# Kernel tuning notes

Measured on AMD Instinct MI355X. Metric: run time of the kernel, lower is better.

Reference implementation:

```python
import jax, jax.numpy as jnp
import numpy as np

# Dims: B=32 batch, C=64 feat channels, Np=192 priors, No=72 row offsets,
# Ns=36 pooled sample points (maxpool kernel 2), Hd=64 fc hidden.
B, C, Np, No, Hd = 32, 64, 192, 72, 64
NS_POOL = 2  # n_offsets // sample_points
REG_DIM = No + 4  # reg_layers output


def bilinear_sample(feat, gx, gy):
    """torch F.grid_sample(align_corners=True) equivalent for in-range coords.
    feat: [B,C,H,W]; gx,gy: [B,Np,S] normalized to [-1,1]. -> [B,C,Np,S]."""
    Bb, Cc, H, W = feat.shape
    ix = (gx + 1.0) * 0.5 * (W - 1)
    iy = (gy + 1.0) * 0.5 * (H - 1)
    ix0f = jnp.floor(ix); iy0f = jnp.floor(iy)
    wx = ix - ix0f; wy = iy - iy0f
    ix0 = jnp.clip(ix0f.astype(jnp.int32), 0, W - 1)
    iy0 = jnp.clip(iy0f.astype(jnp.int32), 0, H - 1)
    ix1 = jnp.clip(ix0 + 1, 0, W - 1)
    iy1 = jnp.clip(iy0 + 1, 0, H - 1)
    ff = feat.reshape(Bb, Cc, H * W)
    S = gx.shape[1] * gx.shape[2]
    def gather(iy_, ix_):
        idx = (iy_ * W + ix_).reshape(Bb, 1, S)
        g = jnp.take_along_axis(ff, jnp.broadcast_to(idx, (Bb, Cc, S)), axis=2)
        return g.reshape(Bb, Cc, gx.shape[1], gx.shape[2])
    v00 = gather(iy0, ix0); v01 = gather(iy0, ix1)
    v10 = gather(iy1, ix0); v11 = gather(iy1, ix1)
    wx = wx[:, None]; wy = wy[:, None]  # broadcast over C
    return (v00 * (1 - wx) * (1 - wy) + v01 * wx * (1 - wy)
            + v10 * (1 - wx) * wy + v11 * wx * wy)


def _mlp2(h, Ws, bs):
    # two stacked Linear+ReLU layers (num_fc=2)
    for i in range(2):
        h = jax.nn.relu(h @ Ws[i] + bs[i])
    return h


def setup_inputs() -> dict:
    key = jax.random.key(0)
    ks = jax.random.split(key, 24)
    w = lambda k, sh: jax.random.normal(k, sh, dtype=jnp.float32) * 0.05
    return {
        "x0": jax.random.normal(ks[0], (B, C, 40, 100), dtype=jnp.float32),
        "x1": jax.random.normal(ks[1], (B, C, 20, 50), dtype=jnp.float32),
        "x2": jax.random.normal(ks[2], (B, C, 10, 25), dtype=jnp.float32),
        "prior_xs0": jax.random.uniform(ks[3], (Np, No), dtype=jnp.float32),
        "l_weight": w(ks[4], (No,)),              # self.l embedding, sigmoid gate
        "lsgi_w": w(ks[5], (3, C, C)),            # per-stage lsgi projection
        "fc_w": w(ks[6], (C, Hd)), "fc_b": w(ks[7], (Hd,)),
        "cls_w": w(ks[8], (2, Hd, Hd)), "cls_b": w(ks[9], (2, Hd)),
        "cls_ow": w(ks[10], (Hd, 2)), "cls_ob": w(ks[11], (2,)),
        "reg_w": w(ks[12], (2, Hd, Hd)), "reg_b": w(ks[13], (2, Hd)),
        "reg_ow": w(ks[14], (Hd, REG_DIM)), "reg_ob": w(ks[15], (REG_DIM,)),
        "loc_w": w(ks[16], (2, Hd, Hd)), "loc_b": w(ks[17], (2, Hd)),
        "loc_ow": w(ks[18], (Hd, 1)), "loc_ob": w(ks[19], (1,)),
    }


def reference(x0, x1, x2, prior_xs0, l_weight, lsgi_w, fc_w, fc_b,
              cls_w, cls_b, cls_ow, cls_ob, reg_w, reg_b, reg_ow, reg_ob,
              loc_w, loc_b, loc_ow, loc_ob):
    pyramid = [x2, x1, x0]  # reversed: coarsest level first (stage 0)
    prior_feat_ys = jnp.linspace(1.0, 0.0, No, dtype=jnp.float32)
    gy = jnp.broadcast_to((prior_feat_ys * 2.0 - 1.0)[None, None, :], (B, Np, No))
    prior_xs = jnp.broadcast_to(prior_xs0[None], (B, Np, No))
    gate = jax.nn.sigmoid(l_weight)[:, None]  # [No,1]
    stage_feats = []
    outs = []
    for s in range(3):
        gx = prior_xs * 2.0 - 1.0
        pooled = bilinear_sample(pyramid[s], gx, gy)          # [B,C,Np,No]
        pooled = jnp.transpose(pooled, (0, 2, 3, 1)) * gate   # [B,Np,No,C]
        pooled = jax.nn.relu(jnp.einsum('bnoc,cd->bnod', pooled, lsgi_w[s]))
        # MaxPool2d kernel (2,1) over the offset axis -> Ns=36 sample points
        comp = pooled.reshape(B, Np, No // NS_POOL, NS_POOL, C).max(axis=3)
        stage_feats.append(comp)
        # cross-stage fusion (global head): mean over stages and sample points
        fused = jnp.stack(stage_feats, 0).mean(axis=0).mean(axis=2)  # [B,Np,C]
        fc = jax.nn.relu(fused @ fc_w + fc_b)                        # [B,Np,Hd]
        cls = _mlp2(fc, cls_w, cls_b) @ cls_ow + cls_ob              # [B,Np,2]
        reg = _mlp2(fc, reg_w, reg_b) @ reg_ow + reg_ob              # [B,Np,No+4]
        loc = _mlp2(fc, loc_w, loc_b) @ loc_ow + loc_ob              # [B,Np,1]
        outs.append(jnp.concatenate([cls, reg, loc], axis=-1))      # [B,Np,79]
        # refine anchors for next stage from predicted xs
        prior_xs = jax.nn.sigmoid(reg[..., 4:])
    return jnp.stack(outs, axis=0)  # [3,B,Np,79]
```

## Files before the change

### kernel.cpp

```cpp
#include <hip/hip_runtime.h>
#include <hip/hip_bf16.h>

#define Bq   32
#define Cq   64
#define NPq  192
#define NOq  72
#define PTS  (NPq * NOq)
#define REGD 76
#define OUTD 79
#define HSTR 68

typedef __attribute__((ext_vector_type(8))) short short8;
typedef __attribute__((ext_vector_type(4))) float float4v;

__device__ inline unsigned short f2bf(float x) {
    __hip_bfloat16 h = __float2bfloat16(x);
    return *reinterpret_cast<unsigned short*>(&h);
}
__device__ inline float bf2f(unsigned short u) {
    unsigned int x = ((unsigned int)u) << 16;
    float f;
    __builtin_memcpy(&f, &x, 4);
    return f;
}

__global__ __launch_bounds__(256) void build_tables_kernel(
    const float* __restrict__ f0,
    const float* __restrict__ f1,
    const float* __restrict__ f2,
    const float* __restrict__ lw,
    unsigned short* __restrict__ t0,
    unsigned short* __restrict__ t1,
    unsigned short* __restrict__ t2)
{
    __shared__ float sRow[64 * 101];

    const int tid = threadIdx.x;
    const int o   = blockIdx.x / 96;
    const int sb  = blockIdx.x - o * 96;
    const int s   = sb >> 5;
    const int b   = sb & 31;

    const float* feat; unsigned short* tab; int H, W;
    if (s == 0)      { feat = f0; tab = t0; H = 10; W = 25; }
    else if (s == 1) { feat = f1; tab = t1; H = 20; W = 50; }
    else             { feat = f2; tab = t2; H = 40; W = 100; }
    const int Wp = W + 1;

    const float ys = 1.0f - (float)o * (1.0f / 71.0f);
    const float iy = ys * (float)(H - 1);
    const float fy = floorf(iy);
    const float wy = iy - fy;
    int iy0 = (int)fy; iy0 = iy0 < 0 ? 0 : (iy0 > H - 1 ? H - 1 : iy0);
    const int iy1 = (iy0 + 1 > H - 1) ? H - 1 : iy0 + 1;
    const float gate = 1.0f / (1.0f + __expf(-lw[o]));

    const float* fb = feat + (size_t)b * 64 * H * W;
    const int iy0W = iy0 * W, iy1W = iy1 * W;

    const int tot = 64 * W;
    for (int idx = tid; idx < tot; idx += 256) {
        const int c = idx / W;
        const int x = idx - c * W;
        const float* f = fb + c * (H * W);
        sRow[c * Wp + x] = ((1.0f - wy) * f[iy0W + x] + wy * f[iy1W + x]) * gate;
    }
    __syncthreads();

    unsigned short* to = tab + (size_t)(b * NOq + o) * Wp * 64;
    const int tot2 = Wp * 64;
    for (int idx = tid; idx < tot2; idx += 256) {
        const int x = idx >> 6;
        const int c = idx & 63;
        const int xx = (x < W) ? x : (W - 1);
        to[idx] = f2bf(sRow[c * Wp + xx]);
    }
}

template<int W>
__global__ __launch_bounds__(256) void fused_pool_kernel(
    const unsigned short* __restrict__ tab,
    const float* __restrict__ xsrc, const int xstride,
    const float* __restrict__ lsgi,
    float* __restrict__ sumFeat,
    const int accumulate)
{
    constexpr int Wp = W + 1;
    const int tid  = threadIdx.x;
    const int w    = tid >> 6;
    const int lane = tid & 63;
    const int ng   = blockIdx.x >> 5;
    const int b    = blockIdx.x & 31;
    const int npair = ng * 4 + w;

    short8 wf[4][2];
    {
        const int kb = ((lane >> 4) & 3) * 8;
        const int dl = lane & 15;
        #pragma unroll
        for (int ks = 0; ks < 2; ++ks)
            #pragma unroll
            for (int dt = 0; dt < 4; ++dt) {
                union { unsigned short u[8]; short8 v; } pk;
                #pragma unroll
                for (int j = 0; j < 8; ++j)
                    pk.u[j] = f2bf(lsgi[(ks * 32 + kb + j) * 64 + dt * 16 + dl]);
                wf[dt][ks] = pk.v;
            }
    }

    const unsigned short* tb = tab + (size_t)b * NOq * Wp * 64;
    const float* xp = xsrc + (size_t)xstride * b;
    const int m  = lane & 15;
    const int kg = lane >> 4;
    const int nt0 = npair * 9;

    float sums0[4] = {0.f, 0.f, 0.f, 0.f};
    float sums1[4] = {0.f, 0.f, 0.f, 0.f};

    #pragma unroll
    for (int ntl = 0; ntl < 9; ++ntl) {
        const int pt = (nt0 + ntl) * 16 + m;
        const int o  = pt % NOq;
        float ixf = xp[pt] * (float)(W - 1);
        ixf = fminf(fmaxf(ixf, 0.0f), (float)(W - 1));
        const float fx = floorf(ixf);
        const float wx = ixf - fx;
        const int ix0 = (int)fx;

        const unsigned short* col = tb + ((size_t)o * Wp + ix0) * 64 + kg * 8;
        union { unsigned short u[8]; short8 v; } t00, t01, t10, t11, a0, a1;
        t00.v = *(const short8*)(col);
        t01.v = *(const short8*)(col + 64);
        t10.v = *(const short8*)(col + 32);
        t11.v = *(const short8*)(col + 96);
        #pragma unroll
        for (int j = 0; j < 8; ++j) {
            const float l0 = bf2f(t00.u[j]), h0 = bf2f(t01.u[j]);
            const float l1 = bf2f(t10.u[j]), h1 = bf2f(t11.u[j]);
            a0.u[j] = f2bf(l0 + wx * (h0 - l0));
            a1.u[j] = f2bf(l1 + wx * (h1 - l1));
        }

        const bool hi = (ntl * 16 + (kg * 4)) >= NOq;
        #pragma unroll
        for (int dt = 0; dt < 4; ++dt) {
            float4v c = {0.f, 0.f, 0.f, 0.f};
            c = __builtin_amdgcn_mfma_f32_16x16x32_bf16(a0.v, wf[dt][0], c, 0, 0, 0);
            c = __builtin_amdgcn_mfma_f32_16x16x32_bf16(a1.v, wf[dt][1], c, 0, 0, 0);
            const float pm0 = fmaxf(fmaxf(c[0], c[1]), 0.f);
            const float pm1 = fmaxf(fmaxf(c[2], c[3]), 0.f);
            const float add = pm0 + pm1;
            if (hi) sums1[dt] += add; else sums0[dt] += add;
        }
    }

    #pragma unroll
    for (int dt = 0; dt < 4; ++dt) {
        float v0 = sums0[dt], v1 = sums1[dt];
        v0 += __shfl_xor(v0, 16); v0 += __shfl_xor(v0, 32);
        v1 += __shfl_xor(v1, 16); v1 += __shfl_xor(v1, 32);
        sums0[dt] = v0; sums1[dt] = v1;
    }

    if (lane < 16) {
        const size_t row0 = (size_t)(b * NPq + npair * 2) * 64;
        #pragma unroll
        for (int dt = 0; dt < 4; ++dt) {
            const int d = dt * 16 + lane;
            float t0 = sums0[dt] * (1.0f / 36.0f);
            float t1 = sums1[dt] * (1.0f / 36.0f);
            float* p0 = sumFeat + row0 + d;
            float* p1 = sumFeat + row0 + 64 + d;
            if (accumulate) { t0 += *p0; t1 += *p1; }
            *p0 = t0; *p1 = t1;
        }
    }
}

__global__ __launch_bounds__(256) void head_kernel(
    const float* __restrict__ sumFeat, const float invS,
    const float* __restrict__ fc_w,  const float* __restrict__ fc_b,
    const float* __restrict__ cls_w, const float* __restrict__ cls_b,
    const float* __restrict__ cls_ow, const float* __restrict__ cls_ob,
    const float* __restrict__ reg_w, const float* __restrict__ reg_b,
    const float* __restrict__ reg_ow, const float* __restrict__ reg_ob,
    const float* __restrict__ loc_w, const float* __restrict__ loc_b,
    const float* __restrict__ loc_ow, const float* __restrict__ loc_ob,
    float* __restrict__ out, float* __restrict__ xs_next)
{
    __shared__ __align__(16) float sAct0[32 * HSTR];
    __shared__ __align__(16) float sAct1[32 * HSTR];
    __shared__ __align__(16) float sW0[4096];
    __shared__ __align__(16) float sW1[4864];

    const int tid = threadIdx.x;
    const int hb  = blockIdx.x % 3;
    const int pg  = blockIdx.x / 3;
    const int p0  = pg * 32;
    const int tm  = tid >> 4;
    const int tn  = tid & 15;

    const float* h_w  = (hb == 0) ? cls_w  : (hb == 1) ? reg_w  : loc_w;
    const float* h_b  = (hb == 0) ? cls_b  : (hb == 1) ? reg_b  : loc_b;
    const float* h_ow = (hb == 0) ? cls_ow : (hb == 1) ? reg_ow : loc_ow;
    const float* h_ob = (hb == 0) ? cls_ob : (hb == 1) ? reg_ob : loc_ob;
    const int ow_n    = (hb == 0) ? 128    : (hb == 1) ? 64 * REGD : 64;

    #pragma unroll
    for (int i = 0; i < 4; ++i)
        *(float4*)&sW0[(i * 256 + tid) * 4] = *(const float4*)&fc_w[(i * 256 + tid) * 4];
    for (int idx = tid; idx < 32 * 64; idx += 256) {
        const int p = idx >> 6, c = idx & 63;
        sAct0[p * HSTR + c] = sumFeat[(size_t)(p0 + p) * 64 + c] * invS;
    }

    auto do_gemm = [&](const float* src, float* dst, const float* wbuf,
                       const float* gb, const float* nextw, int nextn,
                       float* nextbuf) {
        __syncthreads();
        float4 pf[5];
        const int n4 = nextn >> 2;
        #pragma unroll
        for (int i = 0; i < 5; ++i) {
            const int idx = i * 256 + tid;
            if (idx < n4) pf[i] = *(const float4*)&nextw[idx * 4];
        }
        const float4 b4 = *(const float4*)&gb[4 * tn];
        float4 acc0 = b4, acc1 = b4;
        const float* r0 = src + (2 * tm) * HSTR;
        const float* r1 = r0 + HSTR;
        #pragma unroll 4
        for (int k4 = 0; k4 < 16; ++k4) {
            const float4 a0 = *(const float4*)&r0[4 * k4];
            const float4 a1 = *(const float4*)&r1[4 * k4];
            const float4 w0 = *(const float4*)&wbuf[(4 * k4 + 0) * 64 + 4 * tn];
            const float4 w1 = *(const float4*)&wbuf[(4 * k4 + 1) * 64 + 4 * tn];
            const float4 w2 = *(const float4*)&wbuf[(4 * k4 + 2) * 64 + 4 * tn];
            const float4 w3 = *(const float4*)&wbuf[(4 * k4 + 3) * 64 + 4 * tn];
            acc0.x += a0.x*w0.x + a0.y*w1.x + a0.z*w2.x + a0.w*w3.x;
            acc0.y += a0.x*w0.y + a0.y*w1.y + a0.z*w2.y + a0.w*w3.y;
            acc0.z += a0.x*w0.z + a0.y*w1.z + a0.z*w2.z + a0.w*w3.z;
            acc0.w += a0.x*w0.w + a0.y*w1.w + a0.z*w2.w + a0.w*w3.w;
            acc1.x += a1.x*w0.x + a1.y*w1.x + a1.z*w2.x + a1.w*w3.x;
            acc1.y += a1.x*w0.y + a1.y*w1.y + a1.z*w2.y + a1.w*w3.y;
            acc1.z += a1.x*w0.z + a1.y*w1.z + a1.z*w2.z + a1.w*w3.z;
            acc1.w += a1.x*w0.w + a1.y*w1.w + a1.z*w2.w + a1.w*w3.w;
        }
        float4 v0, v1;
        v0.x = fmaxf(acc0.x, 0.f); v0.y = fmaxf(acc0.y, 0.f);
        v0.z = fmaxf(acc0.z, 0.f); v0.w = fmaxf(acc0.w, 0.f);
        v1.x = fmaxf(acc1.x, 0.f); v1.y = fmaxf(acc1.y, 0.f);
        v1.z = fmaxf(acc1.z, 0.f); v1.w = fmaxf(acc1.w, 0.f);
        *(float4*)&dst[(2 * tm) * HSTR + 4 * tn]     = v0;
        *(float4*)&dst[(2 * tm + 1) * HSTR + 4 * tn] = v1;
        #pragma unroll
        for (int i = 0; i < 5; ++i) {
            const int idx = i * 256 + tid;
            if (idx < n4) *(float4*)&nextbuf[idx * 4] = pf[i];
        }
    };

    do_gemm(sAct0, sAct1, sW0, fc_b,      h_w,        4096, sW1);
    do_gemm(sAct1, sAct0, sW1, h_b,       h_w + 4096, 4096, sW0);
    do_gemm(sAct0, sAct1, sW0, h_b + 64,  h_ow,       ow_n, sW1);
    __syncthreads();

    if (hb == 0) {
        if (tid < 64) {
            const int p = tid >> 1, d = tid & 1;
            const float* row = &sAct1[p * HSTR];
            float z = h_ob[d];
            #pragma unroll 4
            for (int k4 = 0; k4 < 16; ++k4) {
                const float4 a = *(const float4*)&row[4 * k4];
                z += a.x * sW1[(4 * k4 + 0) * 2 + d] + a.y * sW1[(4 * k4 + 1) * 2 + d]
                   + a.z * sW1[(4 * k4 + 2) * 2 + d] + a.w * sW1[(4 * k4 + 3) * 2 + d];
            }
            out[(size_t)(p0 + p) * OUTD + d] = z;
        }
    } else if (hb == 1) {
        const int p  = tid & 31;
        const int jg = tid >> 5;
        const float* row = &sAct1[p * HSTR];
        float* orow = out + (size_t)(p0 + p) * OUTD;
        float* xsp  = xs_next + (size_t)(p0 + p) * NOq;
        for (int j = jg; j < REGD; j += 8) {
            float z = h_ob[j];
            #pragma unroll 4
            for (int k4 = 0; k4 < 16; ++k4) {
                const float4 a = *(const float4*)&row[4 * k4];
                z += a.x * sW1[(4 * k4 + 0) * REGD + j] + a.y * sW1[(4 * k4 + 1) * REGD + j]
                   + a.z * sW1[(4 * k4 + 2) * REGD + j] + a.w * sW1[(4 * k4 + 3) * REGD + j];
            }
            orow[2 + j] = z;
            if (j >= 4) xsp[j - 4] = 1.0f / (1.0f + __expf(-z));
        }
    } else {
        if (tid < 32) {
            const float* row = &sAct1[tid * HSTR];
            float z = h_ob[0];
            #pragma unroll 4
            for (int k4 = 0; k4 < 16; ++k4) {
                const float4 a = *(const float4*)&row[4 * k4];
                z += a.x * sW1[4 * k4] + a.y * sW1[4 * k4 + 1]
                   + a.z * sW1[4 * k4 + 2] + a.w * sW1[4 * k4 + 3];
            }
            out[(size_t)(p0 + tid) * OUTD + 78] = z;
        }
    }
}

extern "C" void kernel_launch(void* const* d_in, const int* in_sizes, int n_in,
                              void* d_out, int out_size, void* d_ws, size_t ws_size,
                              hipStream_t stream)
{
    const float* x0        = (const float*)d_in[0];
    const float* x1        = (const float*)d_in[1];
    const float* x2        = (const float*)d_in[2];
    const float* prior_xs0 = (const float*)d_in[3];
    const float* l_weight  = (const float*)d_in[4];
    const float* lsgi_w    = (const float*)d_in[5];
    const float* fc_w      = (const float*)d_in[6];
    const float* fc_b      = (const float*)d_in[7];
    const float* cls_w     = (const float*)d_in[8];
    const float* cls_b     = (const float*)d_in[9];
    const float* cls_ow    = (const float*)d_in[10];
    const float* cls_ob    = (const float*)d_in[11];
    const float* reg_w     = (const float*)d_in[12];
    const float* reg_b     = (const float*)d_in[13];
    const float* reg_ow    = (const float*)d_in[14];
    const float* reg_ob    = (const float*)d_in[15];
    const float* loc_w     = (const float*)d_in[16];
    const float* loc_b     = (const float*)d_in[17];
    const float* loc_ow    = (const float*)d_in[18];
    const float* loc_ob    = (const float*)d_in[19];

    float* out     = (float*)d_out;
    float* sumFeat = (float*)d_ws;
    float* xs      = sumFeat + (size_t)Bq * NPq * Cq;
    unsigned short* tab0 = (unsigned short*)(xs + (size_t)Bq * PTS);
    unsigned short* tab1 = tab0 + (size_t)Bq * NOq * 26  * 64;
    unsigned short* tab2 = tab1 + (size_t)Bq * NOq * 51  * 64;

    hipLaunchKernelGGL(build_tables_kernel, dim3(3 * Bq * NOq), dim3(256), 0, stream,
                       x2, x1, x0, l_weight, tab0, tab1, tab2);

    for (int s = 0; s < 3; ++s) {
        const float* xsrc = (s == 0) ? prior_xs0 : xs;
        const int xstr    = (s == 0) ? 0 : PTS;
        if (s == 0)
            hipLaunchKernelGGL((fused_pool_kernel<25>), dim3(Bq * 24), dim3(256), 0, stream,
                               tab0, xsrc, xstr, lsgi_w + s * 4096, sumFeat, 0);
        else if (s == 1)
            hipLaunchKernelGGL((fused_pool_kernel<50>), dim3(Bq * 24), dim3(256), 0, stream,
                               tab1, xsrc, xstr, lsgi_w + s * 4096, sumFeat, 1);
        else
            hipLaunchKernelGGL((fused_pool_kernel<100>), dim3(Bq * 24), dim3(256), 0, stream,
                               tab2, xsrc, xstr, lsgi_w + s * 4096, sumFeat, 1);

        hipLaunchKernelGGL(head_kernel, dim3((Bq * NPq / 32) * 3), dim3(256), 0, stream,
                           sumFeat, 1.0f / (float)(s + 1),
                           fc_w, fc_b, cls_w, cls_b, cls_ow, cls_ob,
                           reg_w, reg_b, reg_ow, reg_ob,
                           loc_w, loc_b, loc_ow, loc_ob,
                           out + (size_t)s * Bq * NPq * OUTD, xs);
    }
}
```

Baseline: 279.6 us.

## Fuse head MLPs into pooling kernel and template table build on stage dims

The separate head kernel is folded into the pooling kernel: each block keeps its 8 priors' fused features in shared memory and runs the fc, cls, reg and loc MLPs in place. This removes three launches and the sumFeat reload. The table builder is templated on H/W and writes packed bf16 pairs as 32-bit stores. In exchange, each of the 768 blocks reloads every head weight matrix into shared memory for only 8 rows, with many more barriers and serial GEMM phases. It also uses extra shared memory, which may reduce occupancy of the pooling phase.

```diff
diff --git a/kernel.cpp b/kernel.cpp
--- a/kernel.cpp
+++ b/kernel.cpp
@@ -8,7 +8,6 @@
 #define PTS  (NPq * NOq)
 #define REGD 76
 #define OUTD 79
-#define HSTR 68
 
 typedef __attribute__((ext_vector_type(8))) short short8;
 typedef __attribute__((ext_vector_type(4))) float float4v;
@@ -22,6 +21,46 @@
     float f;
     __builtin_memcpy(&f, &x, 4);
     return f;
+}
+
+template<int H, int W>
+__device__ __forceinline__ void build_one(
+    const float* __restrict__ feat, unsigned short* __restrict__ tab,
+    const float* __restrict__ lw, const int b, const int o,
+    float* __restrict__ sRow, const int tid)
+{
+    constexpr int Wp = W + 1;
+
+    const float ys = 1.0f - (float)o * (1.0f / 71.0f);
+    const float iy = ys * (float)(H - 1);
+    const float fy = floorf(iy);
+    const float wy = iy - fy;
+    int iy0 = (int)fy; iy0 = iy0 < 0 ? 0 : (iy0 > H - 1 ? H - 1 : iy0);
+    const int iy1 = (iy0 + 1 > H - 1) ? H - 1 : iy0 + 1;
+    const float gate = 1.0f / (1.0f + __expf(-lw[o]));
+
+    const float* fb = feat + (size_t)b * 64 * H * W;
+    const int iy0W = iy0 * W, iy1W = iy1 * W;
+
+    constexpr int tot = 64 * W;
+    for (int idx = tid; idx < tot; idx += 256) {
+        const int c = idx / W;
+        const int x = idx - c * W;
+        const float* f = fb + c * (H * W);
+        sRow[c * Wp + x] = ((1.0f - wy) * f[iy0W + x] + wy * f[iy1W + x]) * gate;
+    }
+    __syncthreads();
+
+    unsigned int* to = (unsigned int*)(tab + (size_t)(b * NOq + o) * Wp * 64);
+    constexpr int tot2 = Wp * 32;
+    for (int idx = tid; idx < tot2; idx += 256) {
+        const int x  = idx >> 5;
+        const int c0 = (idx & 31) * 2;
+        const int xx = (x < W) ? x : (W - 1);
+        const unsigned int lo = f2bf(sRow[c0 * Wp + xx]);
+        const unsigned int hi = f2bf(sRow[(c0 + 1) * Wp + xx]);
+        to[x * 32 + (c0 >> 1)] = lo | (hi << 16);
+    }
 }
 
 __global__ __launch_bounds__(256) void build_tables_kernel(
@@ -34,58 +73,40 @@
     unsigned short* __restrict__ t2)
 {
     __shared__ float sRow[64 * 101];
-
     const int tid = threadIdx.x;
     const int o   = blockIdx.x / 96;
     const int sb  = blockIdx.x - o * 96;
     const int s   = sb >> 5;
     const int b   = sb & 31;
 
-    const float* feat; unsigned short* tab; int H, W;
-    if (s == 0)      { feat = f0; tab = t0; H = 10; W = 25; }
-    else if (s == 1) { feat = f1; tab = t1; H = 20; W = 50; }
-    else             { feat = f2; tab = t2; H = 40; W = 100; }
-    const int Wp = W + 1;
-
-    const float ys = 1.0f - (float)o * (1.0f / 71.0f);
-    const float iy = ys * (float)(H - 1);
-    const float fy = floorf(iy);
-    const float wy = iy - fy;
-    int iy0 = (int)fy; iy0 = iy0 < 0 ? 0 : (iy0 > H - 1 ? H - 1 : iy0);
-    const int iy1 = (iy0 + 1 > H - 1) ? H - 1 : iy0 + 1;
-    const float gate = 1.0f / (1.0f + __expf(-lw[o]));
-
-    const float* fb = feat + (size_t)b * 64 * H * W;
-    const int iy0W = iy0 * W, iy1W = iy1 * W;
-
-    const int tot = 64 * W;
-    for (int idx = tid; idx < tot; idx += 256) {
-        const int c = idx / W;
-        const int x = idx - c * W;
-        const float* f = fb + c * (H * W);
-        sRow[c * Wp + x] = ((1.0f - wy) * f[iy0W + x] + wy * f[iy1W + x]) * gate;
-    }
-    __syncthreads();
-
-    unsigned short* to = tab + (size_t)(b * NOq + o) * Wp * 64;
-    const int tot2 = Wp * 64;
-    for (int idx = tid; idx < tot2; idx += 256) {
-        const int x = idx >> 6;
-        const int c = idx & 63;
-        const int xx = (x < W) ? x : (W - 1);
-        to[idx] = f2bf(sRow[c * Wp + xx]);
-    }
+    if (s == 0)      build_one<10, 25 >(f0, t0, lw, b, o, sRow, tid);
+    else if (s == 1) build_one<20, 50 >(f1, t1, lw, b, o, sRow, tid);
+    else             build_one<40, 100>(f2, t2, lw, b, o, sRow, tid);
 }
 
 template<int W>
-__global__ __launch_bounds__(256) void fused_pool_kernel(
+__global__ __launch_bounds__(256) void fused_pool_head_kernel(
     const unsigned short* __restrict__ tab,
     const float* __restrict__ xsrc, const int xstride,
     const float* __restrict__ lsgi,
     float* __restrict__ sumFeat,
-    const int accumulate)
+    const int stage,
+    const float* __restrict__ fc_w,  const float* __restrict__ fc_b,
+    const float* __restrict__ cls_w, const float* __restrict__ cls_b,
+    const float* __restrict__ cls_ow, const float* __restrict__ cls_ob,
+    const float* __restrict__ reg_w, const float* __restrict__ reg_b,
+    const float* __restrict__ reg_ow, const float* __restrict__ reg_ob,
+    const float* __restrict__ loc_w, const float* __restrict__ loc_b,
+    const float* __restrict__ loc_ow, const float* __restrict__ loc_ob,
+    float* __restrict__ out, float* __restrict__ xs_next)
 {
     constexpr int Wp = W + 1;
+    __shared__ __align__(16) float sF [8][68];
+    __shared__ __align__(16) float sC [8][68];
+    __shared__ __align__(16) float sT1[8][68];
+    __shared__ __align__(16) float sT2[8][68];
+    __shared__ __align__(16) float sWt[4864];
+
     const int tid  = threadIdx.x;
     const int w    = tid >> 6;
     const int lane = tid & 63;
@@ -163,6 +184,7 @@
         sums0[dt] = v0; sums1[dt] = v1;
     }
 
+    const float invS = 1.0f / (float)(stage + 1);
     if (lane < 16) {
         const size_t row0 = (size_t)(b * NPq + npair * 2) * 64;
         #pragma unroll
@@ -172,142 +194,74 @@
             float t1 = sums1[dt] * (1.0f / 36.0f);
             float* p0 = sumFeat + row0 + d;
             float* p1 = sumFeat + row0 + 64 + d;
-            if (accumulate) { t0 += *p0; t1 += *p1; }
+            if (stage > 0) { t0 += *p0; t1 += *p1; }
             *p0 = t0; *p1 = t1;
-        }
-    }
-}
-
-__global__ __launch_bounds__(256) void head_kernel(
-    const float* __restrict__ sumFeat, const float invS,
-    const float* __restrict__ fc_w,  const float* __restrict__ fc_b,
-    const float* __restrict__ cls_w, const float* __restrict__ cls_b,
-    const float* __restrict__ cls_ow, const float* __restrict__ cls_ob,
-    const float* __restrict__ reg_w, const float* __restrict__ reg_b,
-    const float* __restrict__ reg_ow, const float* __restrict__ reg_ob,
-    const float* __restrict__ loc_w, const float* __restrict__ loc_b,
-    const float* __restrict__ loc_ow, const float* __restrict__ loc_ob,
-    float* __restrict__ out, float* __restrict__ xs_next)
-{
-    __shared__ __align__(16) float sAct0[32 * HSTR];
-    __shared__ __align__(16) float sAct1[32 * HSTR];
-    __shared__ __align__(16) float sW0[4096];
-    __shared__ __align__(16) float sW1[4864];
-
-    const int tid = threadIdx.x;
-    const int hb  = blockIdx.x % 3;
-    const int pg  = blockIdx.x / 3;
-    const int p0  = pg * 32;
-    const int tm  = tid >> 4;
-    const int tn  = tid & 15;
-
-    const float* h_w  = (hb == 0) ? cls_w  : (hb == 1) ? reg_w  : loc_w;
-    const float* h_b  = (hb == 0) ? cls_b  : (hb == 1) ? reg_b  : loc_b;
-    const float* h_ow = (hb == 0) ? cls_ow : (hb == 1) ? reg_ow : loc_ow;
-    const float* h_ob = (hb == 0) ? cls_ob : (hb == 1) ? reg_ob : loc_ob;
-    const int ow_n    = (hb == 0) ? 128    : (hb == 1) ? 64 * REGD : 64;
-
-    #pragma unroll
-    for (int i = 0; i < 4; ++i)
-        *(float4*)&sW0[(i * 256 + tid) * 4] = *(const float4*)&fc_w[(i * 256 + tid) * 4];
-    for (int idx = tid; idx < 32 * 64; idx += 256) {
-        const int p = idx >> 6, c = idx & 63;
-        sAct0[p * HSTR + c] = sumFeat[(size_t)(p0 + p) * 64 + c] * invS;
-    }
-
-    auto do_gemm = [&](const float* src, float* dst, const float* wbuf,
-                       const float* gb, const float* nextw, int nextn,
-                       float* nextbuf) {
+            sF[2 * w][d]     = t0 * invS;
+            sF[2 * w + 1][d] = t1 * invS;
+        }
+    }
+
+    const int pt2 = tid >> 5;
+    const int dh  = tid & 31;
+    const int d0  = dh * 2;
+    const int p0g = b * NPq + ng * 8;
+
+    auto gemm64 = [&](const float (*src)[68], float (*dst)[68],
+                      const float* __restrict__ gw, const float* __restrict__ gb) {
         __syncthreads();
-        float4 pf[5];
-        const int n4 = nextn >> 2;
-        #pragma unroll
-        for (int i = 0; i < 5; ++i) {
-            const int idx = i * 256 + tid;
-            if (idx < n4) pf[i] = *(const float4*)&nextw[idx * 4];
-        }
-        const float4 b4 = *(const float4*)&gb[4 * tn];
-        float4 acc0 = b4, acc1 = b4;
-        const float* r0 = src + (2 * tm) * HSTR;
-        const float* r1 = r0 + HSTR;
-        #pragma unroll 4
-        for (int k4 = 0; k4 < 16; ++k4) {
-            const float4 a0 = *(const float4*)&r0[4 * k4];
-            const float4 a1 = *(const float4*)&r1[4 * k4];
-            const float4 w0 = *(const float4*)&wbuf[(4 * k4 + 0) * 64 + 4 * tn];
-            const float4 w1 = *(const float4*)&wbuf[(4 * k4 + 1) * 64 + 4 * tn];
-            const float4 w2 = *(const float4*)&wbuf[(4 * k4 + 2) * 64 + 4 * tn];
-            const float4 w3 = *(const float4*)&wbuf[(4 * k4 + 3) * 64 + 4 * tn];
-            acc0.x += a0.x*w0.x + a0.y*w1.x + a0.z*w2.x + a0.w*w3.x;
-            acc0.y += a0.x*w0.y + a0.y*w1.y + a0.z*w2.y + a0.w*w3.y;
-            acc0.z += a0.x*w0.z + a0.y*w1.z + a0.z*w2.z + a0.w*w3.z;
-            acc0.w += a0.x*w0.w + a0.y*w1.w + a0.z*w2.w + a0.w*w3.w;
-            acc1.x += a1.x*w0.x + a1.y*w1.x + a1.z*w2.x + a1.w*w3.x;
-            acc1.y += a1.x*w0.y + a1.y*w1.y + a1.z*w2.y + a1.w*w3.y;
-            acc1.z += a1.x*w0.z + a1.y*w1.z + a1.z*w2.z + a1.w*w3.z;
-            acc1.w += a1.x*w0.w + a1.y*w1.w + a1.z*w2.w + a1.w*w3.w;
-        }
-        float4 v0, v1;
-        v0.x = fmaxf(acc0.x, 0.f); v0.y = fmaxf(acc0.y, 0.f);
-        v0.z = fmaxf(acc0.z, 0.f); v0.w = fmaxf(acc0.w, 0.f);
-        v1.x = fmaxf(acc1.x, 0.f); v1.y = fmaxf(acc1.y, 0.f);
-        v1.z = fmaxf(acc1.z, 0.f); v1.w = fmaxf(acc1.w, 0.f);
-        *(float4*)&dst[(2 * tm) * HSTR + 4 * tn]     = v0;
-        *(float4*)&dst[(2 * tm + 1) * HSTR + 4 * tn] = v1;
-        #pragma unroll
-        for (int i = 0; i < 5; ++i) {
-            const int idx = i * 256 + tid;
-            if (idx < n4) *(float4*)&nextbuf[idx * 4] = pf[i];
-        }
+        #pragma unroll
+        for (int i = 0; i < 4; ++i)
+            *(float4*)&sWt[(i * 256 + tid) * 4] = *(const float4*)&gw[(i * 256 + tid) * 4];
+        __syncthreads();
+        float a0 = gb[d0], a1 = gb[d0 + 1];
+        #pragma unroll 8
+        for (int k = 0; k < 64; ++k) {
+            const float av = src[pt2][k];
+            const float2 w2 = *(const float2*)&sWt[k * 64 + d0];
+            a0 += av * w2.x; a1 += av * w2.y;
+        }
+        dst[pt2][d0]     = fmaxf(a0, 0.f);
+        dst[pt2][d0 + 1] = fmaxf(a1, 0.f);
     };
 
-    do_gemm(sAct0, sAct1, sW0, fc_b,      h_w,        4096, sW1);
-    do_gemm(sAct1, sAct0, sW1, h_b,       h_w + 4096, 4096, sW0);
-    do_gemm(sAct0, sAct1, sW0, h_b + 64,  h_ow,       ow_n, sW1);
-    __syncthreads();
-
-    if (hb == 0) {
-        if (tid < 64) {
-            const int p = tid >> 1, d = tid & 1;
-            const float* row = &sAct1[p * HSTR];
-            float z = h_ob[d];
-            #pragma unroll 4
-            for (int k4 = 0; k4 < 16; ++k4) {
-                const float4 a = *(const float4*)&row[4 * k4];
-                z += a.x * sW1[(4 * k4 + 0) * 2 + d] + a.y * sW1[(4 * k4 + 1) * 2 + d]
-                   + a.z * sW1[(4 * k4 + 2) * 2 + d] + a.w * sW1[(4 * k4 + 3) * 2 + d];
-            }
-            out[(size_t)(p0 + p) * OUTD + d] = z;
-        }
-    } else if (hb == 1) {
-        const int p  = tid & 31;
-        const int jg = tid >> 5;
-        const float* row = &sAct1[p * HSTR];
-        float* orow = out + (size_t)(p0 + p) * OUTD;
-        float* xsp  = xs_next + (size_t)(p0 + p) * NOq;
-        for (int j = jg; j < REGD; j += 8) {
-            float z = h_ob[j];
-            #pragma unroll 4
-            for (int k4 = 0; k4 < 16; ++k4) {
-                const float4 a = *(const float4*)&row[4 * k4];
-                z += a.x * sW1[(4 * k4 + 0) * REGD + j] + a.y * sW1[(4 * k4 + 1) * REGD + j]
-                   + a.z * sW1[(4 * k4 + 2) * REGD + j] + a.w * sW1[(4 * k4 + 3) * REGD + j];
-            }
+    gemm64(sF, sC, fc_w, fc_b);
+
+    gemm64(sC,  sT1, cls_w,        cls_b);
+    gemm64(sT1, sT2, cls_w + 4096, cls_b + 64);
+    __syncthreads();
+    if (tid < 16) {
+        const int p = tid >> 1, d = tid & 1;
+        float z = cls_ob[d];
+        #pragma unroll 8
+        for (int k = 0; k < 64; ++k) z += sT2[p][k] * cls_ow[k * 2 + d];
+        out[(size_t)(p0g + p) * OUTD + d] = z;
+    }
+
+    gemm64(sC,  sT1, reg_w,        reg_b);
+    gemm64(sT1, sT2, reg_w + 4096, reg_b + 64);
+    __syncthreads();
+    for (int idx = tid; idx < 64 * REGD; idx += 256) sWt[idx] = reg_ow[idx];
+    __syncthreads();
+    {
+        float* orow = out + (size_t)(p0g + pt2) * OUTD;
+        float* xsp  = xs_next + (size_t)(p0g + pt2) * NOq;
+        for (int j = dh; j < REGD; j += 32) {
+            float z = reg_ob[j];
+            #pragma unroll 8
+            for (int k = 0; k < 64; ++k) z += sT2[pt2][k] * sWt[k * REGD + j];
             orow[2 + j] = z;
             if (j >= 4) xsp[j - 4] = 1.0f / (1.0f + __expf(-z));
         }
-    } else {
-        if (tid < 32) {
-            const float* row = &sAct1[tid * HSTR];
-            float z = h_ob[0];
-            #pragma unroll 4
-            for (int k4 = 0; k4 < 16; ++k4) {
-                const float4 a = *(const float4*)&row[4 * k4];
-                z += a.x * sW1[4 * k4] + a.y * sW1[4 * k4 + 1]
-                   + a.z * sW1[4 * k4 + 2] + a.w * sW1[4 * k4 + 3];
-            }
-            out[(size_t)(p0 + tid) * OUTD + 78] = z;
-        }
+    }
+
+    gemm64(sC,  sT1, loc_w,        loc_b);
+    gemm64(sT1, sT2, loc_w + 4096, loc_b + 64);
+    __syncthreads();
+    if (tid < 8) {
+        float z = loc_ob[0];
+        #pragma unroll 8
+        for (int k = 0; k < 64; ++k) z += sT2[tid][k] * loc_ow[k];
+        out[(size_t)(p0g + tid) * OUTD + 78] = z;
     }
 }
 
@@ -349,21 +303,25 @@
     for (int s = 0; s < 3; ++s) {
         const float* xsrc = (s == 0) ? prior_xs0 : xs;
         const int xstr    = (s == 0) ? 0 : PTS;
+        const unsigned short* tb = (s == 0) ? tab0 : (s == 1) ? tab1 : tab2;
+        float* outS = out + (size_t)s * Bq * NPq * OUTD;
         if (s == 0)
-            hipLaunchKernelGGL((fused_pool_kernel<25>), dim3(Bq * 24), dim3(256), 0, stream,
-                               tab0, xsrc, xstr, lsgi_w + s * 4096, sumFeat, 0);
+            hipLaunchKernelGGL((fused_pool_head_kernel<25>), dim3(Bq * 24), dim3(256), 0, stream,
+                               tb, xsrc, xstr, lsgi_w + s * 4096, sumFeat, s,
+                               fc_w, fc_b, cls_w, cls_b, cls_ow, cls_ob,
+                               reg_w, reg_b, reg_ow, reg_ob,
+                               loc_w, loc_b, loc_ow, loc_ob, outS, xs);
         else if (s == 1)
-            hipLaunchKernelGGL((fused_pool_kernel<50>), dim3(Bq * 24), dim3(256), 0, stream,
-                               tab1, xsrc, xstr, lsgi_w + s * 4096, sumFeat, 1);
+            hipLaunchKernelGGL((fused_pool_head_kernel<50>), dim3(Bq * 24), dim3(256), 0, stream,
+                               tb, xsrc, xstr, lsgi_w + s * 4096, sumFeat, s,
+                               fc_w, fc_b, cls_w, cls_b, cls_ow, cls_ob,
+                               reg_w, reg_b, reg_ow, reg_ob,
+                               loc_w, loc_b, loc_ow, loc_ob, outS, xs);
         else
-            hipLaunchKernelGGL((fused_pool_kernel<100>), dim3(Bq * 24), dim3(256), 0, stream,
-                               tab2, xsrc, xstr, lsgi_w + s * 4096, sumFeat, 1);
-
-        hipLaunchKernelGGL(head_kernel, dim3((Bq * NPq / 32) * 3), dim3(256), 0, stream,
-                           sumFeat, 1.0f / (float)(s + 1),
-                           fc_w, fc_b, cls_w, cls_b, cls_ow, cls_ob,
-                           reg_w, reg_b, reg_ow, reg_ob,
-                           loc_w, loc_b, loc_ow, loc_ob,
-                           out + (size_t)s * Bq * NPq * OUTD, xs);
-    }
-}
+            hipLaunchKernelGGL((fused_pool_head_kernel<100>), dim3(Bq * 24), dim3(256), 0, stream,
+                               tb, xsrc, xstr, lsgi_w + s * 4096, sumFeat, s,
+                               fc_w, fc_b, cls_w, cls_b, cls_ow, cls_ob,
+                               reg_w, reg_b, reg_ow, reg_ob,
+                               loc_w, loc_b, loc_ow, loc_ob, outS, xs);
+    }
+}
```

After: 259.5 us. 7.2% less time.
